# Kernel optimization log

Hardware: AMD Instinct MI355X
Metric: run time of the kernel (lower is better)

Reference implementation:

```python
import jax, jax.numpy as jnp
import numpy as np


def setup_inputs() -> dict:
    key = jax.random.key(0)
    x = jax.random.uniform(key, (8, 3, 224, 224), dtype=jnp.float32)
    return {"x": x, "T": 100}


def reference(x, T):
    # normalize to [0, 1] using global min/max (as in the torch module)
    xn = (x - x.min()) / (x.max() - x.min() + 1e-8)
    # time-to-first-spike index per element, truncated like .long()
    spike_times = jnp.clip(((1.0 - xn) * (T - 1)).astype(jnp.int32), 0, T - 1)  # [B,C,H,W]
    # one-hot along the new time axis: spikes[b, t, ...] = 1 where t == spike_time
    t_axis = jnp.arange(T, dtype=jnp.int32)  # [T]
    spikes = (spike_times[:, None] == t_axis[None, :, None, None, None]).astype(jnp.float32)
    return spikes  # [B, T, C, H, W]
```

## Files before the change

### kernel.cpp

```cpp
#include <hip/hip_runtime.h>
#include <cfloat>

#define BLK 256
#define RED_BLOCKS 256

__global__ void k_minmax_partial(const float* __restrict__ x, int n4,
                                 float* __restrict__ partial) {
    const float4* __restrict__ x4 = (const float4*)x;
    float mn = FLT_MAX, mx = -FLT_MAX;
    for (int i = blockIdx.x * blockDim.x + threadIdx.x; i < n4;
         i += gridDim.x * blockDim.x) {
        float4 v = x4[i];
        mn = fminf(mn, fminf(fminf(v.x, v.y), fminf(v.z, v.w)));
        mx = fmaxf(mx, fmaxf(fmaxf(v.x, v.y), fmaxf(v.z, v.w)));
    }
    for (int off = 32; off > 0; off >>= 1) {
        mn = fminf(mn, __shfl_down(mn, off, 64));
        mx = fmaxf(mx, __shfl_down(mx, off, 64));
    }
    __shared__ float smn[BLK / 64], smx[BLK / 64];
    int lane = threadIdx.x & 63;
    int w = threadIdx.x >> 6;
    if (lane == 0) { smn[w] = mn; smx[w] = mx; }
    __syncthreads();
    if (threadIdx.x == 0) {
        mn = smn[0]; mx = smx[0];
        for (int j = 1; j < BLK / 64; ++j) {
            mn = fminf(mn, smn[j]);
            mx = fmaxf(mx, smx[j]);
        }
        partial[2 * blockIdx.x]     = mn;
        partial[2 * blockIdx.x + 1] = mx;
    }
}

__global__ void k_minmax_final(const float* __restrict__ partial, int nb,
                               float* __restrict__ params) {
    float mn = FLT_MAX, mx = -FLT_MAX;
    for (int i = threadIdx.x; i < nb; i += blockDim.x) {
        mn = fminf(mn, partial[2 * i]);
        mx = fmaxf(mx, partial[2 * i + 1]);
    }
    for (int off = 32; off > 0; off >>= 1) {
        mn = fminf(mn, __shfl_down(mn, off, 64));
        mx = fmaxf(mx, __shfl_down(mx, off, 64));
    }
    __shared__ float smn[BLK / 64], smx[BLK / 64];
    int lane = threadIdx.x & 63;
    int w = threadIdx.x >> 6;
    if (lane == 0) { smn[w] = mn; smx[w] = mx; }
    __syncthreads();
    if (threadIdx.x == 0) {
        mn = smn[0]; mx = smx[0];
        for (int j = 1; j < BLK / 64; ++j) {
            mn = fminf(mn, smn[j]);
            mx = fmaxf(mx, smx[j]);
        }
        params[0] = mn;
        params[1] = (mx - mn) + 1e-8f;
    }
}

__global__ void k_spikes(const float* __restrict__ x,
                         const float* __restrict__ params,
                         const int* __restrict__ Tptr,
                         float* __restrict__ out, int CHW, int n4) {
    int i = blockIdx.x * blockDim.x + threadIdx.x;
    if (i >= n4) return;
    const int T = Tptr[0];
    const float mn = params[0];
    const float d  = params[1];
    const float scaleT = (float)(T - 1);

    float4 v = ((const float4*)x)[i];

    float s0 = (1.0f - (v.x - mn) / d) * scaleT;
    float s1 = (1.0f - (v.y - mn) / d) * scaleT;
    float s2 = (1.0f - (v.z - mn) / d) * scaleT;
    float s3 = (1.0f - (v.w - mn) / d) * scaleT;
    int st0 = (int)s0; st0 = min(max(st0, 0), T - 1);
    int st1 = (int)s1; st1 = min(max(st1, 0), T - 1);
    int st2 = (int)s2; st2 = min(max(st2, 0), T - 1);
    int st3 = (int)s3; st3 = min(max(st3, 0), T - 1);

    int s4 = i * 4;
    int b  = s4 / CHW;
    int r  = s4 - b * CHW;
    float* obase = out + (size_t)b * (size_t)T * (size_t)CHW + (size_t)r;

    for (int t = 0; t < T; ++t) {
        float4 o;
        o.x = (t == st0) ? 1.0f : 0.0f;
        o.y = (t == st1) ? 1.0f : 0.0f;
        o.z = (t == st2) ? 1.0f : 0.0f;
        o.w = (t == st3) ? 1.0f : 0.0f;
        *(float4*)(obase + (size_t)t * (size_t)CHW) = o;
    }
}

extern "C" void kernel_launch(void* const* d_in, const int* in_sizes, int n_in,
                              void* d_out, int out_size, void* d_ws, size_t ws_size,
                              hipStream_t stream) {
    const float* x   = (const float*)d_in[0];
    const int* Tptr  = (const int*)d_in[1];
    float* out       = (float*)d_out;

    const int n  = in_sizes[0];
    const int n4 = n / 4;
    const int B  = 8;
    const int CHW = n / B;

    float* partial = (float*)d_ws;
    float* params  = partial + 2 * RED_BLOCKS;

    k_minmax_partial<<<RED_BLOCKS, BLK, 0, stream>>>(x, n4, partial);
    k_minmax_final<<<1, BLK, 0, stream>>>(partial, RED_BLOCKS, params);

    int blocks = (n4 + BLK - 1) / BLK;
    k_spikes<<<blocks, BLK, 0, stream>>>(x, params, Tptr, out, CHW, n4);
}
```

Baseline: 478.2 us.

## Precompute byte spike times then write one-hot output plane by plane

Splits the spike kernel in two. The first pass stores each element's spike time as a byte in workspace. The second pass launches one block per (batch, time, split) segment, so every block streams contiguous float4 stores across a single output plane instead of each thread striding through all T planes. This is meant to improve write locality and parallelism for the store-bound output. The cost is an extra launch and re-reading the byte array T times, and T is now hard-coded to 100 on the host.

```diff
diff --git a/kernel.cpp b/kernel.cpp
--- a/kernel.cpp
+++ b/kernel.cpp
@@ -3,6 +3,7 @@
 
 #define BLK 256
 #define RED_BLOCKS 256
+#define SPLIT 7
 
 __global__ void k_minmax_partial(const float* __restrict__ x, int n4,
                                  float* __restrict__ partial) {
@@ -61,10 +62,10 @@
     }
 }
 
-__global__ void k_spikes(const float* __restrict__ x,
-                         const float* __restrict__ params,
-                         const int* __restrict__ Tptr,
-                         float* __restrict__ out, int CHW, int n4) {
+__global__ void k_spiketime(const float* __restrict__ x,
+                            const float* __restrict__ params,
+                            const int* __restrict__ Tptr,
+                            unsigned char* __restrict__ st, int n4) {
     int i = blockIdx.x * blockDim.x + threadIdx.x;
     if (i >= n4) return;
     const int T = Tptr[0];
@@ -73,49 +74,75 @@
     const float scaleT = (float)(T - 1);
 
     float4 v = ((const float4*)x)[i];
+    int st0 = (int)((1.0f - (v.x - mn) / d) * scaleT);
+    int st1 = (int)((1.0f - (v.y - mn) / d) * scaleT);
+    int st2 = (int)((1.0f - (v.z - mn) / d) * scaleT);
+    int st3 = (int)((1.0f - (v.w - mn) / d) * scaleT);
+    st0 = min(max(st0, 0), T - 1);
+    st1 = min(max(st1, 0), T - 1);
+    st2 = min(max(st2, 0), T - 1);
+    st3 = min(max(st3, 0), T - 1);
 
-    float s0 = (1.0f - (v.x - mn) / d) * scaleT;
-    float s1 = (1.0f - (v.y - mn) / d) * scaleT;
-    float s2 = (1.0f - (v.z - mn) / d) * scaleT;
-    float s3 = (1.0f - (v.w - mn) / d) * scaleT;
-    int st0 = (int)s0; st0 = min(max(st0, 0), T - 1);
-    int st1 = (int)s1; st1 = min(max(st1, 0), T - 1);
-    int st2 = (int)s2; st2 = min(max(st2, 0), T - 1);
-    int st3 = (int)s3; st3 = min(max(st3, 0), T - 1);
+    uchar4 o;
+    o.x = (unsigned char)st0;
+    o.y = (unsigned char)st1;
+    o.z = (unsigned char)st2;
+    o.w = (unsigned char)st3;
+    ((uchar4*)st)[i] = o;
+}
 
-    int s4 = i * 4;
-    int b  = s4 / CHW;
-    int r  = s4 - b * CHW;
-    float* obase = out + (size_t)b * (size_t)T * (size_t)CHW + (size_t)r;
+__global__ void k_write(const unsigned char* __restrict__ st,
+                        float* __restrict__ out,
+                        int T, int CHW4, int PC) {
+    int seg   = blockIdx.x;
+    int part  = seg % SPLIT;
+    int plane = seg / SPLIT;
+    int t = plane % T;
+    int b = plane / T;
 
-    for (int t = 0; t < T; ++t) {
+    const uchar4* __restrict__ stp = (const uchar4*)st + (size_t)b * CHW4;
+    float4* __restrict__ op = (float4*)out + (size_t)plane * CHW4;
+
+    int jbeg = part * PC + threadIdx.x;
+    int jend = min((part + 1) * PC, CHW4);
+
+    #pragma unroll 3
+    for (int j = jbeg; j < jend; j += BLK) {
+        uchar4 s = stp[j];
         float4 o;
-        o.x = (t == st0) ? 1.0f : 0.0f;
-        o.y = (t == st1) ? 1.0f : 0.0f;
-        o.z = (t == st2) ? 1.0f : 0.0f;
-        o.w = (t == st3) ? 1.0f : 0.0f;
-        *(float4*)(obase + (size_t)t * (size_t)CHW) = o;
+        o.x = (s.x == t) ? 1.0f : 0.0f;
+        o.y = (s.y == t) ? 1.0f : 0.0f;
+        o.z = (s.z == t) ? 1.0f : 0.0f;
+        o.w = (s.w == t) ? 1.0f : 0.0f;
+        op[j] = o;
     }
 }
 
 extern "C" void kernel_launch(void* const* d_in, const int* in_sizes, int n_in,
                               void* d_out, int out_size, void* d_ws, size_t ws_size,
                               hipStream_t stream) {
-    const float* x   = (const float*)d_in[0];
-    const int* Tptr  = (const int*)d_in[1];
-    float* out       = (float*)d_out;
+    const float* x  = (const float*)d_in[0];
+    const int* Tptr = (const int*)d_in[1];
+    float* out      = (float*)d_out;
 
     const int n  = in_sizes[0];
     const int n4 = n / 4;
     const int B  = 8;
-    const int CHW = n / B;
+    const int T  = 100;
+    const int CHW  = n / B;
+    const int CHW4 = CHW / 4;
+    const int PC   = (CHW4 + SPLIT - 1) / SPLIT;
 
-    float* partial = (float*)d_ws;
-    float* params  = partial + 2 * RED_BLOCKS;
+    float* partial     = (float*)d_ws;
+    float* params      = partial + 2 * RED_BLOCKS;
+    unsigned char* st  = (unsigned char*)d_ws + 4096;
 
     k_minmax_partial<<<RED_BLOCKS, BLK, 0, stream>>>(x, n4, partial);
     k_minmax_final<<<1, BLK, 0, stream>>>(partial, RED_BLOCKS, params);
 
     int blocks = (n4 + BLK - 1) / BLK;
-    k_spikes<<<blocks, BLK, 0, stream>>>(x, params, Tptr, out, CHW, n4);
+    k_spiketime<<<blocks, BLK, 0, stream>>>(x, params, Tptr, st, n4);
+
+    int wblocks = B * T * SPLIT;
+    k_write<<<wblocks, BLK, 0, stream>>>(st, out, T, CHW4, PC);
 }
```

Result: no change. 484.1 us (+1.2%).
